# Kernel optimization log

Hardware: AMD Instinct MI355X
Metric: run time of the kernel (lower is better)

Reference implementation:

```python
import jax, jax.numpy as jnp
import numpy as np
import math

# model dims
B, S, T = 4, 256, 8
D_MODEL, D_STATE, N_HEAD, NUM_LAYERS = 256, 128, 4, 2
VOCAB = 32000
D_HEAD = D_STATE // N_HEAD
# AdaptiveLIFNeuron constants
TAU, BASE_THR, ADAPT, TARGET = 2.0, 1.0, 0.1, 0.02
DECAY = math.exp(-1.0 / TAU)


@jax.custom_vjp
def spike_fn(x):
    # spikingjelly surrogate.ATan forward = heaviside
    return (x >= 0).astype(x.dtype)

def _spike_fwd(x):
    return spike_fn(x), x

def _spike_bwd(x, g):
    # ATan surrogate gradient, alpha=2: 1 / (1 + (pi*x)^2)
    return (g / (1.0 + (math.pi * x) ** 2),)

spike_fn.defvjp(_spike_fwd, _spike_bwd)


def lif_step(x, v, thr):
    v_pot = v * DECAY + x
    spike = spike_fn(v_pot - jax.lax.stop_gradient(thr))
    v_new = v_pot * (1.0 - jax.lax.stop_gradient(spike))  # reset where spiked
    err = jax.lax.stop_gradient(spike.mean() - TARGET)    # torch.no_grad threshold update
    thr_new = jnp.maximum(thr + ADAPT * err, 0.5)
    return spike, v_new, thr_new


def ssm_layer(x_tbsd, A, C, Wq, bq, Wkv, bkv, Wo, bo):
    # x_tbsd: [T, B, S, d_model] spikes/embeddings, scanned over time
    scale = 1.0 / math.sqrt(D_HEAD)

    def step(carry, x_t):
        h, sv, ov, ts, to = carry
        st = h @ A.T                                      # [B,S,d_state]
        q = (h @ Wq.T + bq).reshape(B * S, N_HEAD, D_HEAD)
        kv = x_t @ Wkv.T + bkv                            # [B,S,2*d_state]
        k, v = jnp.split(kv, 2, axis=-1)
        k = k.reshape(B * S, N_HEAD, D_HEAD)
        v = v.reshape(B * S, N_HEAD, D_HEAD)
        # attention across all B*S positions (faithful to torch reshape)
        scores = jnp.einsum('ahd,bhd->hab', q, k) * scale  # [H, BS, BS]
        attn = jax.nn.softmax(scores, axis=-1)
        att = jnp.einsum('hab,bhd->ahd', attn, v).reshape(B, S, D_STATE)
        upd = st + att @ Wo.T + bo
        h2, sv2, ts2 = lif_step(upd, sv, ts)
        out_pot = h2 @ C.T                                 # [B,S,d_model]
        os_, ov2, to2 = lif_step(out_pot, ov, to)
        return (h2, sv2, ov2, ts2, to2), os_

    init = (jnp.zeros((B, S, D_STATE)), jnp.zeros((B, S, D_STATE)),
            jnp.zeros((B, S, D_MODEL)),
            jnp.full((D_STATE,), BASE_THR), jnp.full((D_MODEL,), BASE_THR))
    _, outs = jax.lax.scan(step, init, x_tbsd)
    return outs  # [T,B,S,d_model]


def setup_inputs() -> dict:
    key = jax.random.key(0)
    ks = jax.random.split(key, 8)
    nrm = lambda k, shape, s: jax.random.normal(k, shape, jnp.float32) * s
    L = NUM_LAYERS
    return {
        'input_ids': jax.random.randint(ks[0], (B, S), 0, VOCAB),
        'emb': nrm(ks[1], (VOCAB, D_MODEL), 0.02),
        'A': nrm(ks[2], (L, D_STATE, D_STATE), 1.0 / math.sqrt(D_STATE)),
        'C': nrm(ks[3], (L, D_MODEL, D_STATE), 1.0 / math.sqrt(D_STATE)),
        'Wq': nrm(ks[4], (L, D_STATE, D_STATE), 1.0 / math.sqrt(D_STATE)),
        'bq': jnp.zeros((L, D_STATE)),
        'Wkv': nrm(ks[5], (L, 2 * D_STATE, D_MODEL), 1.0 / math.sqrt(D_MODEL)),
        'bkv': jnp.zeros((L, 2 * D_STATE)),
        'Wo': nrm(ks[6], (L, D_STATE, D_STATE), 1.0 / math.sqrt(D_STATE)),
        'bo': jnp.zeros((L, D_STATE)),
        'Wout': nrm(ks[7], (VOCAB, D_MODEL), 1.0 / math.sqrt(D_MODEL)),
        'bout': jnp.zeros((VOCAB,)),
    }


def reference(input_ids, emb, A, C, Wq, bq, Wkv, bkv, Wo, bo, Wout, bout):
    tok = emb[input_ids]                                   # [B,S,d_model]
    # encoder_type='expand': replicate embedding over time steps
    hidden = jnp.broadcast_to(tok[None], (T, B, S, D_MODEL))
    for l in range(NUM_LAYERS):
        hidden = ssm_layer(hidden, A[l], C[l], Wq[l], bq[l],
                           Wkv[l], bkv[l], Wo[l], bo[l])
    time_integrated = hidden.mean(axis=0)                  # mean over time -> [B,S,d_model]
    logits = time_integrated @ Wout.T + bout               # output_projection -> [B,S,vocab]
    return logits
```

## Files before the change

### kernel.cpp

```cpp
#include <hip/hip_runtime.h>
#include <math.h>

#define BS_TOT   1024
#define DM       256
#define DST      128
#define TSTEPS   8
#define DECAYF   0.6065306597126334f
#define SCALEF   0.17677669529663689f
#define NE       (BS_TOT * DM)

__global__ void embed_k(const int* __restrict__ ids, const float* __restrict__ emb,
                        float* __restrict__ tok) {
    int r = blockIdx.x, c = threadIdx.x;
    tok[r * DM + c] = emb[(size_t)ids[r] * DM + c];
}

__global__ void prep_k(float* __restrict__ h, float* __restrict__ sv, float* __restrict__ ov,
                       float* __restrict__ W1T, float* __restrict__ WoT, float* __restrict__ CT,
                       const float* __restrict__ Al, const float* __restrict__ Wql,
                       const float* __restrict__ Wol, const float* __restrict__ Cl,
                       int* __restrict__ cnts) {
    int i = blockIdx.x * 256 + threadIdx.x;
    if (i < BS_TOT * DST) { h[i] = 0.f; sv[i] = 0.f; }
    ov[i] = 0.f;
    if (i < 32768) {
        int k = i >> 8, n = i & 255;
        W1T[i] = (n < 128) ? Al[n * 128 + k] : Wql[(n - 128) * 128 + k];
        CT[i]  = Cl[n * 128 + k];
    }
    if (i < 16384) {
        int k = i >> 7, n = i & 127;
        WoT[i] = Wol[n * 128 + k];
    }
    if (i < 16) cnts[i] = 0;
}

__global__ __launch_bounds__(256) void ktrans_k(const float* __restrict__ kv,
                                                float* __restrict__ kT) {
    __shared__ float tile[64][133];
    const float* src = kv + (size_t)blockIdx.y * NE;
    float* dst = kT + (size_t)blockIdx.y * (128 * 1024);
    const int kc = blockIdx.x, tid = threadIdx.x;
#pragma unroll
    for (int i = 0; i < 32; ++i) {
        int idx = i * 256 + tid;
        int key = idx >> 7, d = idx & 127;
        tile[key][d] = src[(size_t)(kc * 64 + key) * 256 + d];
    }
    __syncthreads();
#pragma unroll
    for (int i = 0; i < 32; ++i) {
        int idx = i * 256 + tid;
        int d = idx >> 6, key = idx & 63;
        dst[(size_t)d * 1024 + kc * 64 + key] = tile[key][d];
    }
}

__global__ void mean_k(const float* __restrict__ outs, float* __restrict__ ti) {
    int i = blockIdx.x * 256 + threadIdx.x;
    float s = 0.f;
#pragma unroll
    for (int t = 0; t < TSTEPS; ++t) s += outs[t * NE + i];
    ti[i] = s * 0.125f;
}

template <int BM, int BN, int BK, int TM, int TN>
__global__ __launch_bounds__((BM / TM) * (BN / TN))
void gemm_k(const float* __restrict__ Amat, const float* __restrict__ Wmat,
            const float* __restrict__ bias, float* __restrict__ outp,
            int M, int N, int K) {
    constexpr int NT  = (BM / TM) * (BN / TN);
    constexpr int NXT = BN / TN;
    __shared__ float As[BK][BM + 4];
    __shared__ float Bs[BK][BN + 4];
    const int tid = threadIdx.x;
    const int n0 = blockIdx.x * BN, m0 = blockIdx.y * BM;
    const int tx = tid % NXT, ty = tid / NXT;
    float acc[TM][TN] = {};

    for (int k0 = 0; k0 < K; k0 += BK) {
#pragma unroll
        for (int i = 0; i < (BM * BK) / NT; ++i) {
            int idx = i * NT + tid;
            int kk = idx % BK, mm = idx / BK;
            As[kk][mm] = Amat[(size_t)(m0 + mm) * K + k0 + kk];
        }
#pragma unroll
        for (int i = 0; i < (BN * BK) / NT; ++i) {
            int idx = i * NT + tid;
            int kk = idx % BK, nn = idx / BK;
            Bs[kk][nn] = Wmat[(size_t)(n0 + nn) * K + k0 + kk];
        }
        __syncthreads();
#pragma unroll
        for (int kk = 0; kk < BK; ++kk) {
            float a[TM], b[TN];
#pragma unroll
            for (int i = 0; i < TM; ++i) a[i] = As[kk][ty * TM + i];
#pragma unroll
            for (int j = 0; j < TN; ++j) b[j] = Bs[kk][tx * TN + j];
#pragma unroll
            for (int i = 0; i < TM; ++i)
#pragma unroll
                for (int j = 0; j < TN; ++j) acc[i][j] += a[i] * b[j];
        }
        __syncthreads();
    }
#pragma unroll
    for (int i = 0; i < TM; ++i) {
        int mr = m0 + ty * TM + i;
#pragma unroll
        for (int j = 0; j < TN; ++j) {
            int nc = n0 + tx * TN + j;
            float x = acc[i][j];
            if (bias) x += bias[nc];
            outp[(size_t)mr * N + nc] = x;
        }
    }
}

__global__ __launch_bounds__(256) void gemm_out_k(
    const float* __restrict__ Amat, const float* __restrict__ Wmat,
    const float* __restrict__ bias, float* __restrict__ outp)
{
    constexpr int BM = 128, BN = 128, BK = 16;
    constexpr int K = 256, N = 32000;
    __shared__ float As[BK][BM + 4];
    __shared__ float Bs[BK][BN + 4];
    const int tid = threadIdx.x;

    const int bid = blockIdx.x;
    const int g   = (bid & 7) * 250 + (bid >> 3);
    const int m0  = (g & 7) * BM;
    const int n0  = (g >> 3) * BN;

    const int tx = tid & 15, ty = tid >> 4;
    float acc[8][8] = {};

    for (int k0 = 0; k0 < K; k0 += BK) {
#pragma unroll
        for (int i = 0; i < 8; ++i) {
            int idx = i * 256 + tid;
            int kk = idx & 15, mm = idx >> 4;
            As[kk][mm] = Amat[(size_t)(m0 + mm) * K + k0 + kk];
        }
#pragma unroll
        for (int i = 0; i < 8; ++i) {
            int idx = i * 256 + tid;
            int kk = idx & 15, nn = idx >> 4;
            Bs[kk][nn] = Wmat[(size_t)(n0 + nn) * K + k0 + kk];
        }
        __syncthreads();
#pragma unroll
        for (int kk = 0; kk < BK; ++kk) {
            float a[8], b[8];
            *(float4*)&a[0] = *(const float4*)&As[kk][ty * 4];
            *(float4*)&a[4] = *(const float4*)&As[kk][64 + ty * 4];
            *(float4*)&b[0] = *(const float4*)&Bs[kk][tx * 4];
            *(float4*)&b[4] = *(const float4*)&Bs[kk][64 + tx * 4];
#pragma unroll
            for (int i = 0; i < 8; ++i)
#pragma unroll
                for (int j = 0; j < 8; ++j) acc[i][j] += a[i] * b[j];
        }
        __syncthreads();
    }

    float bv[8];
    *(float4*)&bv[0] = *(const float4*)&bias[n0 + tx * 4];
    *(float4*)&bv[4] = *(const float4*)&bias[n0 + 64 + tx * 4];
#pragma unroll
    for (int i = 0; i < 8; ++i) {
        const int mr = m0 + ((i < 4) ? (ty * 4 + i) : (64 + ty * 4 + i - 4));
        float4 o0, o1;
        o0.x = acc[i][0] + bv[0]; o0.y = acc[i][1] + bv[1];
        o0.z = acc[i][2] + bv[2]; o0.w = acc[i][3] + bv[3];
        o1.x = acc[i][4] + bv[4]; o1.y = acc[i][5] + bv[5];
        o1.z = acc[i][6] + bv[6]; o1.w = acc[i][7] + bv[7];
        float* dst = &outp[(size_t)mr * N + n0];
        *(float4*)(dst + tx * 4)      = o0;
        *(float4*)(dst + 64 + tx * 4) = o1;
    }
}

__global__ __launch_bounds__(256) void lif_k(
    const float* __restrict__ W1T,
    const float* __restrict__ WoT,
    const float* __restrict__ CT,
    const float* __restrict__ bq_w,
    const float* __restrict__ bo_w,
    float* __restrict__ h,
    float* __restrict__ sv,
    float* __restrict__ ov,
    const float* __restrict__ att_in,
    float* __restrict__ outs_prev,
    float* __restrict__ q_g,
    int* __restrict__ cnt1, int* __restrict__ cnt2, int t, int do_B)
{
    __shared__ float hA_s[4 * 128];
    __shared__ float h2_s[4 * 128];
    __shared__ float att_s[4 * 128];
    __shared__ unsigned long long umr_s[4][2];
    __shared__ unsigned long long um_s[2];
    __shared__ float thr_s[2];

    const int tid = threadIdx.x;
    const int r0 = blockIdx.x * 4;

    if (tid == 0) {
        float ts = 1.0f, to = 1.0f;
        for (int i = 0; i < t - 1; ++i) {
            float e1 = (float)cnt1[i] * (1.f / 131072.f) - 0.02f;
            ts = fmaxf(ts + 0.1f * e1, 0.5f);
            float e2 = (float)cnt2[i] * (1.f / 262144.f) - 0.02f;
            to = fmaxf(to + 0.1f * e2, 0.5f);
        }
        thr_s[0] = ts; thr_s[1] = to;
    }
    hA_s[tid]       = h[r0 * 128 + tid];
    hA_s[256 + tid] = h[r0 * 128 + 256 + tid];
    if (t > 0) {
        att_s[tid]       = att_in[r0 * 128 + tid];
        att_s[256 + tid] = att_in[r0 * 128 + 256 + tid];
    }
    __syncthreads();
    {
        int w = tid >> 6, l = tid & 63;
        unsigned long long b0 = __ballot(hA_s[w * 128 + l] != 0.f);
        unsigned long long b1 = __ballot(hA_s[w * 128 + 64 + l] != 0.f);
        if (l == 0) { umr_s[w][0] = b0; umr_s[w][1] = b1; }
    }
    __syncthreads();
    if (tid == 0) {
        um_s[0] = umr_s[0][0] | umr_s[1][0] | umr_s[2][0] | umr_s[3][0];
        um_s[1] = umr_s[0][1] | umr_s[1][1] | umr_s[2][1] | umr_s[3][1];
    }
    __syncthreads();

    const int n = tid & 127, half = tid >> 7;
    const int ra = half * 2, rb = half * 2 + 1;

    if (t > 0) {
        float sta = 0.f, stb = 0.f;
        unsigned long long u = um_s[0];
        while (u) {
            int k = __builtin_ctzll(u); u &= u - 1;
            float w = W1T[(k << 8) + n];
            sta += hA_s[ra * 128 + k] * w; stb += hA_s[rb * 128 + k] * w;
        }
        u = um_s[1];
        while (u) {
            int kk = __builtin_ctzll(u); u &= u - 1;
            int k = 64 + kk;
            float w = W1T[(k << 8) + n];
            sta += hA_s[ra * 128 + k] * w; stb += hA_s[rb * 128 + k] * w;
        }
        float ba = 0.f, bb = 0.f;
        for (int i4 = 0; i4 < 32; ++i4) {
            const int i = i4 * 4;
            float w0 = WoT[(i + 0) * 128 + n];
            float w1 = WoT[(i + 1) * 128 + n];
            float w2 = WoT[(i + 2) * 128 + n];
            float w3 = WoT[(i + 3) * 128 + n];
            float4 aa = *(const float4*)&att_s[ra * 128 + i];
            float4 ab = *(const float4*)&att_s[rb * 128 + i];
            ba += aa.x * w0; ba += aa.y * w1; ba += aa.z * w2; ba += aa.w * w3;
            bb += ab.x * w0; bb += ab.y * w1; bb += ab.z * w2; bb += ab.w * w3;
        }
        float ts = thr_s[0];
        float xa = ba + bo_w[n]; xa += sta;
        float va = sv[(r0 + ra) * 128 + n];
        float vpa = va * DECAYF + xa;
        float spa = (vpa - ts >= 0.f) ? 1.f : 0.f;
        h[(r0 + ra) * 128 + n]  = spa;
        sv[(r0 + ra) * 128 + n] = vpa * (1.f - spa);
        h2_s[ra * 128 + n] = spa;

        float xb = bb + bo_w[n]; xb += stb;
        float vb = sv[(r0 + rb) * 128 + n];
        float vpb = vb * DECAYF + xb;
        float spb = (vpb - ts >= 0.f) ? 1.f : 0.f;
        h[(r0 + rb) * 128 + n]  = spb;
        sv[(r0 + rb) * 128 + n] = vpb * (1.f - spb);
        h2_s[rb * 128 + n] = spb;

        unsigned long long bba = __ballot(spa != 0.f);
        unsigned long long bbb = __ballot(spb != 0.f);
        int w = tid >> 6, l = tid & 63;
        if (l == 0) {
            umr_s[ra][w & 1] = bba;
            umr_s[rb][w & 1] = bbb;
            atomicAdd(&cnt1[t - 1], __popcll(bba) + __popcll(bbb));
        }
    } else {
        h2_s[tid]       = hA_s[tid];
        h2_s[256 + tid] = hA_s[256 + tid];
    }
    __syncthreads();
    if (tid == 0) {
        um_s[0] = umr_s[0][0] | umr_s[1][0] | umr_s[2][0] | umr_s[3][0];
        um_s[1] = umr_s[0][1] | umr_s[1][1] | umr_s[2][1] | umr_s[3][1];
    }
    __syncthreads();

    if (t > 0) {
        const int n2 = tid;
        float a0 = 0.f, a1 = 0.f, a2 = 0.f, a3 = 0.f;
        unsigned long long u = um_s[0];
        while (u) {
            int k = __builtin_ctzll(u); u &= u - 1;
            float w = CT[(k << 8) + n2];
            a0 += h2_s[k] * w;       a1 += h2_s[128 + k] * w;
            a2 += h2_s[256 + k] * w; a3 += h2_s[384 + k] * w;
        }
        u = um_s[1];
        while (u) {
            int kk = __builtin_ctzll(u); u &= u - 1;
            int k = 64 + kk;
            float w = CT[(k << 8) + n2];
            a0 += h2_s[k] * w;       a1 += h2_s[128 + k] * w;
            a2 += h2_s[256 + k] * w; a3 += h2_s[384 + k] * w;
        }
        float to = thr_s[1];
        float accs[4] = {a0, a1, a2, a3};
        float sp[4];
#pragma unroll
        for (int r = 0; r < 4; ++r) {
            float vo = ov[(r0 + r) * 256 + n2];
            float vp = vo * DECAYF + accs[r];
            float s = (vp - to >= 0.f) ? 1.f : 0.f;
            sp[r] = s;
            outs_prev[(size_t)(r0 + r) * 256 + n2] = s;
            ov[(r0 + r) * 256 + n2] = vp * (1.f - s);
        }
        unsigned long long c0 = __ballot(sp[0] != 0.f);
        unsigned long long c1 = __ballot(sp[1] != 0.f);
        unsigned long long c2 = __ballot(sp[2] != 0.f);
        unsigned long long c3 = __ballot(sp[3] != 0.f);
        if ((tid & 63) == 0)
            atomicAdd(&cnt2[t - 1], __popcll(c0) + __popcll(c1) + __popcll(c2) + __popcll(c3));
    }

    if (do_B) {
        float qa = 0.f, qb = 0.f;
        unsigned long long u = um_s[0];
        while (u) {
            int k = __builtin_ctzll(u); u &= u - 1;
            float w = W1T[(k << 8) + 128 + n];
            qa += h2_s[ra * 128 + k] * w; qb += h2_s[rb * 128 + k] * w;
        }
        u = um_s[1];
        while (u) {
            int kk = __builtin_ctzll(u); u &= u - 1;
            int k = 64 + kk;
            float w = W1T[(k << 8) + 128 + n];
            qa += h2_s[ra * 128 + k] * w; qb += h2_s[rb * 128 + k] * w;
        }
        q_g[(r0 + ra) * 128 + n] = qa + bq_w[n];
        q_g[(r0 + rb) * 128 + n] = qb + bq_w[n];
    }
}

__global__ __launch_bounds__(256) void attn_k(
    const float* __restrict__ q_g,
    const float* __restrict__ kT,
    const float* __restrict__ kv,
    float* __restrict__ att_out)
{
    __shared__ float p_s[8][1032];
    __shared__ float v_s[2][64 * 32];
    __shared__ float q_s[8][32];
    __shared__ float red_s[8 * 33];
    __shared__ float mrow_s[8], linv_s[8];

    const int tid = threadIdx.x;
    const int hh = blockIdx.x >> 7;
    const int r0 = (blockIdx.x & 127) * 8;

    {
        int r = tid >> 5, d = tid & 31;
        q_s[r][d] = q_g[(size_t)(r0 + r) * 128 + hh * 32 + d];
    }
    __syncthreads();

    {
        const int w = tid >> 6, l = tid & 63;
        const int key4 = w * 64 + l;
        const float4* kT4 = (const float4*)(kT + (size_t)hh * 32 * 1024);
        float4 acc[8];
#pragma unroll
        for (int pass = 0; pass < 2; ++pass) {
            const int d0 = pass * 16;
            float4 kreg[16];
#pragma unroll
            for (int i = 0; i < 16; ++i) kreg[i] = kT4[(size_t)(d0 + i) * 256 + key4];
#pragma unroll
            for (int r = 0; r < 8; ++r)
                acc[r] = pass ? *(const float4*)&p_s[r][key4 * 4]
                              : make_float4(0.f, 0.f, 0.f, 0.f);
#pragma unroll
            for (int i4 = 0; i4 < 4; ++i4) {
#pragma unroll
                for (int r = 0; r < 8; ++r) {
                    float4 qv = *(const float4*)&q_s[r][d0 + i4 * 4];
                    float4 k0 = kreg[i4 * 4 + 0], k1 = kreg[i4 * 4 + 1];
                    float4 k2 = kreg[i4 * 4 + 2], k3 = kreg[i4 * 4 + 3];
                    acc[r].x += qv.x * k0.x; acc[r].x += qv.y * k1.x;
                    acc[r].x += qv.z * k2.x; acc[r].x += qv.w * k3.x;
                    acc[r].y += qv.x * k0.y; acc[r].y += qv.y * k1.y;
                    acc[r].y += qv.z * k2.y; acc[r].y += qv.w * k3.y;
                    acc[r].z += qv.x * k0.z; acc[r].z += qv.y * k1.z;
                    acc[r].z += qv.z * k2.z; acc[r].z += qv.w * k3.z;
                    acc[r].w += qv.x * k0.w; acc[r].w += qv.y * k1.w;
                    acc[r].w += qv.z * k2.w; acc[r].w += qv.w * k3.w;
                }
            }
            if (pass == 0) {
#pragma unroll
                for (int r = 0; r < 8; ++r)
                    *(float4*)&p_s[r][key4 * 4] = acc[r];
            } else {
#pragma unroll
                for (int r = 0; r < 8; ++r) {
                    acc[r].x *= SCALEF; acc[r].y *= SCALEF;
                    acc[r].z *= SCALEF; acc[r].w *= SCALEF;
                    *(float4*)&p_s[r][key4 * 4] = acc[r];
                }
            }
        }
    }
    __syncthreads();

    {
        const int rh = tid >> 5, lg = tid & 31;
        float mx = -1e30f;
        for (int jj = 0; jj < 32; ++jj) mx = fmaxf(mx, p_s[rh][lg + 32 * jj]);
        red_s[rh * 33 + lg] = mx;
        __syncthreads();
        if (tid < 8) {
            float m = red_s[tid * 33];
            for (int j = 1; j < 32; ++j) m = fmaxf(m, red_s[tid * 33 + j]);
            mrow_s[tid] = m;
        }
        __syncthreads();
        float m = mrow_s[rh];
        float ls = 0.f;
        for (int jj = 0; jj < 32; ++jj) {
            int a = lg + 32 * jj;
            float p = expf(p_s[rh][a] - m);
            p_s[rh][a] = p;
            ls += p;
        }
        red_s[rh * 33 + lg] = ls;
        __syncthreads();
        if (tid < 8) {
            float l = 0.f;
            for (int j = 0; j < 32; ++j) l += red_s[tid * 33 + j];
            linv_s[tid] = 1.0f / l;
        }
    }
    __syncthreads();

    {
        const int w = tid >> 6, l = tid & 63;
        const int r = l >> 3, dq = l & 7;
        const bool act = (w == 0);
        const float4* kv4 = (const float4*)kv;
        float4 stg0, stg1;
        {
            int i0 = tid, i1 = 256 + tid;
            stg0 = kv4[(size_t)(i0 >> 3) * 64 + 32 + hh * 8 + (i0 & 7)];
            stg1 = kv4[(size_t)(i1 >> 3) * 64 + 32 + hh * 8 + (i1 & 7)];
        }
        float4 a = make_float4(0.f, 0.f, 0.f, 0.f);
        for (int c = 0; c < 16; ++c) {
            float* vb = v_s[c & 1];
            *(float4*)&vb[tid * 4]        = stg0;
            *(float4*)&vb[1024 + tid * 4] = stg1;
            if (c < 15) {
                int i0 = tid, i1 = 256 + tid;
                stg0 = kv4[(size_t)((c + 1) * 64 + (i0 >> 3)) * 64 + 32 + hh * 8 + (i0 & 7)];
                stg1 = kv4[(size_t)((c + 1) * 64 + (i1 >> 3)) * 64 + 32 + hh * 8 + (i1 & 7)];
            }
            __syncthreads();
            if (act) {
#pragma unroll 4
                for (int k4 = 0; k4 < 16; ++k4) {
                    const int kb = k4 * 4;
                    float4 p4 = *(const float4*)&p_s[r][c * 64 + kb];
                    float4 v0 = *(const float4*)&vb[(kb + 0) * 32 + dq * 4];
                    float4 v1 = *(const float4*)&vb[(kb + 1) * 32 + dq * 4];
                    float4 v2 = *(const float4*)&vb[(kb + 2) * 32 + dq * 4];
                    float4 v3 = *(const float4*)&vb[(kb + 3) * 32 + dq * 4];
                    a.x += p4.x * v0.x; a.y += p4.x * v0.y; a.z += p4.x * v0.z; a.w += p4.x * v0.w;
                    a.x += p4.y * v1.x; a.y += p4.y * v1.y; a.z += p4.y * v1.z; a.w += p4.y * v1.w;
                    a.x += p4.z * v2.x; a.y += p4.z * v2.y; a.z += p4.z * v2.z; a.w += p4.z * v2.w;
                    a.x += p4.w * v3.x; a.y += p4.w * v3.y; a.z += p4.w * v3.z; a.w += p4.w * v3.w;
                }
            }
        }
        if (act) {
            float li = linv_s[r];
            a.x *= li; a.y *= li; a.z *= li; a.w *= li;
            *(float4*)&att_out[(size_t)(r0 + r) * 128 + hh * 32 + dq * 4] = a;
        }
    }
}

extern "C" void kernel_launch(void* const* d_in, const int* in_sizes, int n_in,
                              void* d_out, int out_size, void* d_ws, size_t ws_size,
                              hipStream_t stream) {
    (void)in_sizes; (void)n_in; (void)out_size; (void)ws_size;
    const int*   ids  = (const int*)d_in[0];
    const float* emb  = (const float*)d_in[1];
    const float* Aw   = (const float*)d_in[2];
    const float* Cw   = (const float*)d_in[3];
    const float* Wq   = (const float*)d_in[4];
    const float* bq   = (const float*)d_in[5];
    const float* Wkv  = (const float*)d_in[6];
    const float* bkv  = (const float*)d_in[7];
    const float* Wo   = (const float*)d_in[8];
    const float* bo   = (const float*)d_in[9];
    const float* Wout = (const float*)d_in[10];
    const float* bout = (const float*)d_in[11];
    float* out = (float*)d_out;
    float* ws  = (float*)d_ws;

    float* tok  = ws;
    float* bufA = tok  + NE;
    float* bufB = bufA + 8 * NE;
    float* kvb  = bufB + 8 * NE;
    float* kTb  = kvb  + 8 * NE;
    float* attb = kTb  + 8 * 131072;
    float* hbuf = attb + 131072;
    float* svb  = hbuf + 131072;
    float* ovb  = svb  + 131072;
    float* qg   = ovb  + 262144;
    float* ti   = qg   + 131072;
    float* W1T  = ti   + NE;
    float* WoT  = W1T  + 32768;
    float* CT   = WoT  + 16384;
    int*   cnts = (int*)(CT + 32768);

    embed_k<<<dim3(1024), dim3(256), 0, stream>>>(ids, emb, tok);

    for (int l = 0; l < 2; ++l) {
        const float* Al   = Aw  + l * 16384;
        const float* Cl   = Cw  + l * 32768;
        const float* Wql  = Wq  + l * 16384;
        const float* bql  = bq  + l * 128;
        const float* Wkvl = Wkv + l * 65536;
        const float* bkvl = bkv + l * 256;
        const float* Wol  = Wo  + l * 16384;
        const float* bol  = bo  + l * 128;
        const float* xin  = (l == 0) ? tok : bufA;
        float* outs       = (l == 0) ? bufA : bufB;
        const int Mkv     = (l == 0) ? BS_TOT : 8 * BS_TOT;
        const int nt      = (l == 0) ? 1 : 8;

        prep_k<<<dim3(1024), dim3(256), 0, stream>>>(hbuf, svb, ovb, W1T, WoT, CT,
                                                     Al, Wql, Wol, Cl, cnts);

        gemm_k<64, 64, 16, 4, 4><<<dim3(256 / 64, Mkv / 64), dim3(256), 0, stream>>>(
            xin, Wkvl, bkvl, kvb, Mkv, 256, 256);

        ktrans_k<<<dim3(16, nt), dim3(256), 0, stream>>>(kvb, kTb);

        for (int t = 0; t <= TSTEPS; ++t) {
            const int do_B = (t < TSTEPS) ? 1 : 0;
            float* outs_prev = outs + (size_t)((t > 0) ? (t - 1) : 0) * NE;
            lif_k<<<dim3(256), dim3(256), 0, stream>>>(
                W1T, WoT, CT, bql, bol,
                hbuf, svb, ovb, attb, outs_prev, qg,
                cnts, cnts + 8, t, do_B);
            if (do_B) {
                const float* kT_t = (l == 0) ? kTb : kTb + (size_t)t * 131072;
                const float* kv_t = (l == 0) ? kvb : kvb + (size_t)t * NE;
                attn_k<<<dim3(512), dim3(256), 0, stream>>>(qg, kT_t, kv_t, attb);
            }
        }
    }

    mean_k<<<dim3(1024), dim3(256), 0, stream>>>(bufB, ti);

    gemm_out_k<<<dim3(2000), dim3(256), 0, stream>>>(ti, Wout, bout, out);
}
```

Before: 1.271 ms.

## Double-buffer output GEMM and software-pipeline sparse spike-driven matvec loops

The vocab output GEMM now uses two shared-memory buffers and register prefetch, so global loads for the next K tile overlap the FMA work on the current tile, and one barrier per iteration is removed. The sparse bitmask-driven loops in the recurrent kernel load the next weight one iteration ahead to hide memory latency. The C and Wq sparse products are merged into a single loop over the active mask so it is walked once. The cost is more registers and shared memory, which may lower occupancy, and the merged loop now runs even when t==0 or do_B is false.

```diff
diff --git a/kernel.cpp b/kernel.cpp
--- a/kernel.cpp
+++ b/kernel.cpp
@@ -125,8 +125,8 @@
 {
     constexpr int BM = 128, BN = 128, BK = 16;
     constexpr int K = 256, N = 32000;
-    __shared__ float As[BK][BM + 4];
-    __shared__ float Bs[BK][BN + 4];
+    __shared__ float As[2][BK][BM + 4];
+    __shared__ float Bs[2][BK][BN + 4];
     const int tid = threadIdx.x;
 
     const int bid = blockIdx.x;
@@ -136,34 +136,59 @@
 
     const int tx = tid & 15, ty = tid >> 4;
     float acc[8][8] = {};
-
-    for (int k0 = 0; k0 < K; k0 += BK) {
-#pragma unroll
-        for (int i = 0; i < 8; ++i) {
-            int idx = i * 256 + tid;
-            int kk = idx & 15, mm = idx >> 4;
-            As[kk][mm] = Amat[(size_t)(m0 + mm) * K + k0 + kk];
-        }
-#pragma unroll
-        for (int i = 0; i < 8; ++i) {
-            int idx = i * 256 + tid;
-            int kk = idx & 15, nn = idx >> 4;
-            Bs[kk][nn] = Wmat[(size_t)(n0 + nn) * K + k0 + kk];
-        }
-        __syncthreads();
+    float ra_[8], rb_[8];
+
+#pragma unroll
+    for (int i = 0; i < 8; ++i) {
+        int idx = i * 256 + tid;
+        int kk = idx & 15, mm = idx >> 4;
+        ra_[i] = Amat[(size_t)(m0 + mm) * K + kk];
+        rb_[i] = Wmat[(size_t)(n0 + mm) * K + kk];
+    }
+#pragma unroll
+    for (int i = 0; i < 8; ++i) {
+        int idx = i * 256 + tid;
+        int kk = idx & 15, mm = idx >> 4;
+        As[0][kk][mm] = ra_[i];
+        Bs[0][kk][mm] = rb_[i];
+    }
+    __syncthreads();
+
+    int p = 0;
+    for (int k0 = BK; k0 <= K; k0 += BK) {
+        const bool pf = (k0 < K);
+        if (pf) {
+#pragma unroll
+            for (int i = 0; i < 8; ++i) {
+                int idx = i * 256 + tid;
+                int kk = idx & 15, mm = idx >> 4;
+                ra_[i] = Amat[(size_t)(m0 + mm) * K + k0 + kk];
+                rb_[i] = Wmat[(size_t)(n0 + mm) * K + k0 + kk];
+            }
+        }
 #pragma unroll
         for (int kk = 0; kk < BK; ++kk) {
             float a[8], b[8];
-            *(float4*)&a[0] = *(const float4*)&As[kk][ty * 4];
-            *(float4*)&a[4] = *(const float4*)&As[kk][64 + ty * 4];
-            *(float4*)&b[0] = *(const float4*)&Bs[kk][tx * 4];
-            *(float4*)&b[4] = *(const float4*)&Bs[kk][64 + tx * 4];
+            *(float4*)&a[0] = *(const float4*)&As[p][kk][ty * 4];
+            *(float4*)&a[4] = *(const float4*)&As[p][kk][64 + ty * 4];
+            *(float4*)&b[0] = *(const float4*)&Bs[p][kk][tx * 4];
+            *(float4*)&b[4] = *(const float4*)&Bs[p][kk][64 + tx * 4];
 #pragma unroll
             for (int i = 0; i < 8; ++i)
 #pragma unroll
                 for (int j = 0; j < 8; ++j) acc[i][j] += a[i] * b[j];
         }
-        __syncthreads();
+        if (pf) {
+#pragma unroll
+            for (int i = 0; i < 8; ++i) {
+                int idx = i * 256 + tid;
+                int kk = idx & 15, mm = idx >> 4;
+                As[p ^ 1][kk][mm] = ra_[i];
+                Bs[p ^ 1][kk][mm] = rb_[i];
+            }
+            __syncthreads();
+            p ^= 1;
+        }
     }
 
     float bv[8];
@@ -242,18 +267,27 @@
 
     if (t > 0) {
         float sta = 0.f, stb = 0.f;
-        unsigned long long u = um_s[0];
-        while (u) {
-            int k = __builtin_ctzll(u); u &= u - 1;
-            float w = W1T[(k << 8) + n];
-            sta += hA_s[ra * 128 + k] * w; stb += hA_s[rb * 128 + k] * w;
-        }
-        u = um_s[1];
-        while (u) {
-            int kk = __builtin_ctzll(u); u &= u - 1;
-            int k = 64 + kk;
-            float w = W1T[(k << 8) + n];
-            sta += hA_s[ra * 128 + k] * w; stb += hA_s[rb * 128 + k] * w;
+        {
+            unsigned long long u = um_s[0];
+            int kp = 0; float wp = 0.f; bool have = (u != 0ull);
+            if (have) { kp = __builtin_ctzll(u); u &= u - 1; wp = W1T[(kp << 8) + n]; }
+            while (u) {
+                int kn = __builtin_ctzll(u); u &= u - 1;
+                float wn = W1T[(kn << 8) + n];
+                sta += hA_s[ra * 128 + kp] * wp; stb += hA_s[rb * 128 + kp] * wp;
+                kp = kn; wp = wn;
+            }
+            if (have) { sta += hA_s[ra * 128 + kp] * wp; stb += hA_s[rb * 128 + kp] * wp; }
+            u = um_s[1];
+            have = (u != 0ull);
+            if (have) { kp = 64 + __builtin_ctzll(u); u &= u - 1; wp = W1T[(kp << 8) + n]; }
+            while (u) {
+                int kn = 64 + __builtin_ctzll(u); u &= u - 1;
+                float wn = W1T[(kn << 8) + n];
+                sta += hA_s[ra * 128 + kp] * wp; stb += hA_s[rb * 128 + kp] * wp;
+                kp = kn; wp = wn;
+            }
+            if (have) { sta += hA_s[ra * 128 + kp] * wp; stb += hA_s[rb * 128 + kp] * wp; }
         }
         float ba = 0.f, bb = 0.f;
         for (int i4 = 0; i4 < 32; ++i4) {
@@ -303,61 +337,75 @@
     }
     __syncthreads();
 
-    if (t > 0) {
+    {
         const int n2 = tid;
-        float a0 = 0.f, a1 = 0.f, a2 = 0.f, a3 = 0.f;
+        float a0 = 0.f, a1 = 0.f, a2 = 0.f, a3 = 0.f, qa = 0.f, qb = 0.f;
         unsigned long long u = um_s[0];
+        int kp = 0; float wc = 0.f, wq = 0.f; bool have = (u != 0ull);
+        if (have) {
+            kp = __builtin_ctzll(u); u &= u - 1;
+            wc = CT[(kp << 8) + n2]; wq = W1T[(kp << 8) + 128 + n];
+        }
         while (u) {
-            int k = __builtin_ctzll(u); u &= u - 1;
-            float w = CT[(k << 8) + n2];
-            a0 += h2_s[k] * w;       a1 += h2_s[128 + k] * w;
-            a2 += h2_s[256 + k] * w; a3 += h2_s[384 + k] * w;
+            int kn = __builtin_ctzll(u); u &= u - 1;
+            float wcn = CT[(kn << 8) + n2];
+            float wqn = W1T[(kn << 8) + 128 + n];
+            a0 += h2_s[kp] * wc;       a1 += h2_s[128 + kp] * wc;
+            a2 += h2_s[256 + kp] * wc; a3 += h2_s[384 + kp] * wc;
+            qa += h2_s[ra * 128 + kp] * wq; qb += h2_s[rb * 128 + kp] * wq;
+            kp = kn; wc = wcn; wq = wqn;
+        }
+        if (have) {
+            a0 += h2_s[kp] * wc;       a1 += h2_s[128 + kp] * wc;
+            a2 += h2_s[256 + kp] * wc; a3 += h2_s[384 + kp] * wc;
+            qa += h2_s[ra * 128 + kp] * wq; qb += h2_s[rb * 128 + kp] * wq;
         }
         u = um_s[1];
+        have = (u != 0ull);
+        if (have) {
+            kp = 64 + __builtin_ctzll(u); u &= u - 1;
+            wc = CT[(kp << 8) + n2]; wq = W1T[(kp << 8) + 128 + n];
+        }
         while (u) {
-            int kk = __builtin_ctzll(u); u &= u - 1;
-            int k = 64 + kk;
-            float w = CT[(k << 8) + n2];
-            a0 += h2_s[k] * w;       a1 += h2_s[128 + k] * w;
-            a2 += h2_s[256 + k] * w; a3 += h2_s[384 + k] * w;
-        }
-        float to = thr_s[1];
-        float accs[4] = {a0, a1, a2, a3};
-        float sp[4];
-#pragma unroll
-        for (int r = 0; r < 4; ++r) {
-            float vo = ov[(r0 + r) * 256 + n2];
-            float vp = vo * DECAYF + accs[r];
-            float s = (vp - to >= 0.f) ? 1.f : 0.f;
-            sp[r] = s;
-            outs_prev[(size_t)(r0 + r) * 256 + n2] = s;
-            ov[(r0 + r) * 256 + n2] = vp * (1.f - s);
-        }
-        unsigned long long c0 = __ballot(sp[0] != 0.f);
-        unsigned long long c1 = __ballot(sp[1] != 0.f);
-        unsigned long long c2 = __ballot(sp[2] != 0.f);
-        unsigned long long c3 = __ballot(sp[3] != 0.f);
-        if ((tid & 63) == 0)
-            atomicAdd(&cnt2[t - 1], __popcll(c0) + __popcll(c1) + __popcll(c2) + __popcll(c3));
-    }
-
-    if (do_B) {
-        float qa = 0.f, qb = 0.f;
-        unsigned long long u = um_s[0];
-        while (u) {
-            int k = __builtin_ctzll(u); u &= u - 1;
-            float w = W1T[(k << 8) + 128 + n];
-            qa += h2_s[ra * 128 + k] * w; qb += h2_s[rb * 128 + k] * w;
-        }
-        u = um_s[1];
-        while (u) {
-            int kk = __builtin_ctzll(u); u &= u - 1;
-            int k = 64 + kk;
-            float w = W1T[(k << 8) + 128 + n];
-            qa += h2_s[ra * 128 + k] * w; qb += h2_s[rb * 128 + k] * w;
-        }
-        q_g[(r0 + ra) * 128 + n] = qa + bq_w[n];
-        q_g[(r0 + rb) * 128 + n] = qb + bq_w[n];
+            int kn = 64 + __builtin_ctzll(u); u &= u - 1;
+            float wcn = CT[(kn << 8) + n2];
+            float wqn = W1T[(kn << 8) + 128 + n];
+            a0 += h2_s[kp] * wc;       a1 += h2_s[128 + kp] * wc;
+            a2 += h2_s[256 + kp] * wc; a3 += h2_s[384 + kp] * wc;
+            qa += h2_s[ra * 128 + kp] * wq; qb += h2_s[rb * 128 + kp] * wq;
+            kp = kn; wc = wcn; wq = wqn;
+        }
+        if (have) {
+            a0 += h2_s[kp] * wc;       a1 += h2_s[128 + kp] * wc;
+            a2 += h2_s[256 + kp] * wc; a3 += h2_s[384 + kp] * wc;
+            qa += h2_s[ra * 128 + kp] * wq; qb += h2_s[rb * 128 + kp] * wq;
+        }
+
+        if (t > 0) {
+            float to = thr_s[1];
+            float accs[4] = {a0, a1, a2, a3};
+            float sp[4];
+#pragma unroll
+            for (int r = 0; r < 4; ++r) {
+                float vo = ov[(r0 + r) * 256 + n2];
+                float vp = vo * DECAYF + accs[r];
+                float s = (vp - to >= 0.f) ? 1.f : 0.f;
+                sp[r] = s;
+                outs_prev[(size_t)(r0 + r) * 256 + n2] = s;
+                ov[(r0 + r) * 256 + n2] = vp * (1.f - s);
+            }
+            unsigned long long c0 = __ballot(sp[0] != 0.f);
+            unsigned long long c1 = __ballot(sp[1] != 0.f);
+            unsigned long long c2 = __ballot(sp[2] != 0.f);
+            unsigned long long c3 = __ballot(sp[3] != 0.f);
+            if ((tid & 63) == 0)
+                atomicAdd(&cnt2[t - 1], __popcll(c0) + __popcll(c1) + __popcll(c2) + __popcll(c3));
+        }
+
+        if (do_B) {
+            q_g[(r0 + ra) * 128 + n] = qa + bq_w[n];
+            q_g[(r0 + rb) * 128 + n] = qb + bq_w[n];
+        }
     }
 }
 
```

Result: slower. 1.395 ms (+9.8%).

## Use direct global-to-LDS loads with swizzle in vocab GEMM; spread P·V over two waves

Applied to the files above, without the earlier changes.

The output-projection GEMM now stages A and W tiles with global_load_lds 16-byte direct-to-LDS transfers into a K-contiguous, XOR-swizzled layout with BK=32, replacing the register-staged transposed stores. The inner loop reads float4 along K and unpacks four k-steps at a time. Separately, the attention P·V accumulation now uses two waves with two outputs per thread instead of one wave with four, to raise parallelism in that phase. The swizzle is meant to avoid LDS bank conflicts, but the loads are still not double-buffered.

```diff
diff --git a/kernel.cpp b/kernel.cpp
--- a/kernel.cpp
+++ b/kernel.cpp
@@ -8,6 +8,11 @@
 #define DECAYF   0.6065306597126334f
 #define SCALEF   0.17677669529663689f
 #define NE       (BS_TOT * DM)
+
+#define GLOAD_LDS16(g, l) \
+    __builtin_amdgcn_global_load_lds( \
+        (const __attribute__((address_space(1))) void*)(g), \
+        (__attribute__((address_space(3))) void*)(l), 16, 0, 0)
 
 __global__ void embed_k(const int* __restrict__ ids, const float* __restrict__ emb,
                         float* __restrict__ tok) {
@@ -123,45 +128,60 @@
     const float* __restrict__ Amat, const float* __restrict__ Wmat,
     const float* __restrict__ bias, float* __restrict__ outp)
 {
-    constexpr int BM = 128, BN = 128, BK = 16;
     constexpr int K = 256, N = 32000;
-    __shared__ float As[BK][BM + 4];
-    __shared__ float Bs[BK][BN + 4];
+    __shared__ float As2[128 * 32];
+    __shared__ float Bs2[128 * 32];
     const int tid = threadIdx.x;
 
     const int bid = blockIdx.x;
     const int g   = (bid & 7) * 250 + (bid >> 3);
-    const int m0  = (g & 7) * BM;
-    const int n0  = (g >> 3) * BN;
+    const int m0  = (g & 7) * 128;
+    const int n0  = (g >> 3) * 128;
 
     const int tx = tid & 15, ty = tid >> 4;
     float acc[8][8] = {};
 
-    for (int k0 = 0; k0 < K; k0 += BK) {
-#pragma unroll
-        for (int i = 0; i < 8; ++i) {
+    const int swa = ty & 7;
+    const int swb = tx & 7;
+
+    for (int k0 = 0; k0 < K; k0 += 32) {
+#pragma unroll
+        for (int i = 0; i < 4; ++i) {
             int idx = i * 256 + tid;
-            int kk = idx & 15, mm = idx >> 4;
-            As[kk][mm] = Amat[(size_t)(m0 + mm) * K + k0 + kk];
-        }
-#pragma unroll
-        for (int i = 0; i < 8; ++i) {
-            int idx = i * 256 + tid;
-            int kk = idx & 15, nn = idx >> 4;
-            Bs[kk][nn] = Wmat[(size_t)(n0 + nn) * K + k0 + kk];
+            int row = idx >> 3, k4 = idx & 7;
+            int k4s = k4 ^ ((row >> 2) & 7);
+            GLOAD_LDS16(&Amat[(size_t)(m0 + row) * K + k0 + k4s * 4], &As2[idx * 4]);
+            GLOAD_LDS16(&Wmat[(size_t)(n0 + row) * K + k0 + k4s * 4], &Bs2[idx * 4]);
         }
         __syncthreads();
-#pragma unroll
-        for (int kk = 0; kk < BK; ++kk) {
-            float a[8], b[8];
-            *(float4*)&a[0] = *(const float4*)&As[kk][ty * 4];
-            *(float4*)&a[4] = *(const float4*)&As[kk][64 + ty * 4];
-            *(float4*)&b[0] = *(const float4*)&Bs[kk][tx * 4];
-            *(float4*)&b[4] = *(const float4*)&Bs[kk][64 + tx * 4];
-#pragma unroll
-            for (int i = 0; i < 8; ++i)
-#pragma unroll
-                for (int j = 0; j < 8; ++j) acc[i][j] += a[i] * b[j];
+
+#pragma unroll
+        for (int kg = 0; kg < 8; ++kg) {
+            const int pa = (kg ^ swa) * 4;
+            const int pb = (kg ^ swb) * 4;
+            float4 a0[4], a1[4], b0[4], b1[4];
+#pragma unroll
+            for (int i = 0; i < 4; ++i) {
+                a0[i] = *(const float4*)&As2[(ty * 4 + i) * 32 + pa];
+                a1[i] = *(const float4*)&As2[(64 + ty * 4 + i) * 32 + pa];
+                b0[i] = *(const float4*)&Bs2[(tx * 4 + i) * 32 + pb];
+                b1[i] = *(const float4*)&Bs2[(64 + tx * 4 + i) * 32 + pb];
+            }
+#pragma unroll
+            for (int kk2 = 0; kk2 < 4; ++kk2) {
+                float a[8], b[8];
+#pragma unroll
+                for (int i = 0; i < 4; ++i) {
+                    a[i]     = ((const float*)&a0[i])[kk2];
+                    a[4 + i] = ((const float*)&a1[i])[kk2];
+                    b[i]     = ((const float*)&b0[i])[kk2];
+                    b[4 + i] = ((const float*)&b1[i])[kk2];
+                }
+#pragma unroll
+                for (int i = 0; i < 8; ++i)
+#pragma unroll
+                    for (int j = 0; j < 8; ++j) acc[i][j] += a[i] * b[j];
+            }
         }
         __syncthreads();
     }
@@ -463,8 +483,9 @@
 
     {
         const int w = tid >> 6, l = tid & 63;
-        const int r = l >> 3, dq = l & 7;
-        const bool act = (w == 0);
+        const int r = (w & 1) * 4 + (l >> 4);
+        const int dp = l & 15;
+        const bool act = (w < 2);
         const float4* kv4 = (const float4*)kv;
         float4 stg0, stg1;
         {
@@ -472,7 +493,7 @@
             stg0 = kv4[(size_t)(i0 >> 3) * 64 + 32 + hh * 8 + (i0 & 7)];
             stg1 = kv4[(size_t)(i1 >> 3) * 64 + 32 + hh * 8 + (i1 & 7)];
         }
-        float4 a = make_float4(0.f, 0.f, 0.f, 0.f);
+        float a0 = 0.f, a1 = 0.f;
         for (int c = 0; c < 16; ++c) {
             float* vb = v_s[c & 1];
             *(float4*)&vb[tid * 4]        = stg0;
@@ -488,21 +509,21 @@
                 for (int k4 = 0; k4 < 16; ++k4) {
                     const int kb = k4 * 4;
                     float4 p4 = *(const float4*)&p_s[r][c * 64 + kb];
-                    float4 v0 = *(const float4*)&vb[(kb + 0) * 32 + dq * 4];
-                    float4 v1 = *(const float4*)&vb[(kb + 1) * 32 + dq * 4];
-                    float4 v2 = *(const float4*)&vb[(kb + 2) * 32 + dq * 4];
-                    float4 v3 = *(const float4*)&vb[(kb + 3) * 32 + dq * 4];
-                    a.x += p4.x * v0.x; a.y += p4.x * v0.y; a.z += p4.x * v0.z; a.w += p4.x * v0.w;
-                    a.x += p4.y * v1.x; a.y += p4.y * v1.y; a.z += p4.y * v1.z; a.w += p4.y * v1.w;
-                    a.x += p4.z * v2.x; a.y += p4.z * v2.y; a.z += p4.z * v2.z; a.w += p4.z * v2.w;
-                    a.x += p4.w * v3.x; a.y += p4.w * v3.y; a.z += p4.w * v3.z; a.w += p4.w * v3.w;
+                    float2 v0 = *(const float2*)&vb[(kb + 0) * 32 + 2 * dp];
+                    float2 v1 = *(const float2*)&vb[(kb + 1) * 32 + 2 * dp];
+                    float2 v2 = *(const float2*)&vb[(kb + 2) * 32 + 2 * dp];
+                    float2 v3 = *(const float2*)&vb[(kb + 3) * 32 + 2 * dp];
+                    a0 += p4.x * v0.x; a1 += p4.x * v0.y;
+                    a0 += p4.y * v1.x; a1 += p4.y * v1.y;
+                    a0 += p4.z * v2.x; a1 += p4.z * v2.y;
+                    a0 += p4.w * v3.x; a1 += p4.w * v3.y;
                 }
             }
         }
         if (act) {
             float li = linv_s[r];
-            a.x *= li; a.y *= li; a.z *= li; a.w *= li;
-            *(float4*)&att_out[(size_t)(r0 + r) * 128 + hh * 32 + dq * 4] = a;
+            *(float2*)&att_out[(size_t)(r0 + r) * 128 + hh * 32 + 2 * dp] =
+                make_float2(a0 * li, a1 * li);
         }
     }
 }
```

Result: no change. 1.295 ms (+1.9%).

## Widen output GEMM K-tile with float4 loads and spread attention PV across two waves

Applied to the files above, without the earlier changes.

The vocab projection GEMM now uses a K tile of 32 and loads A and W tiles with float4 global reads, halving the number of K iterations and barriers. In the attention kernel, QK accumulators stay in registers across both passes instead of round-tripping through shared memory. The PV stage now runs on two waves, each thread producing two outputs, using a single padded V buffer with an extra barrier per chunk in place of double buffering. Shared memory per GEMM block roughly doubles, and the added barrier may expose the global load latency for V.

```diff
diff --git a/kernel.cpp b/kernel.cpp
--- a/kernel.cpp
+++ b/kernel.cpp
@@ -123,7 +123,7 @@
     const float* __restrict__ Amat, const float* __restrict__ Wmat,
     const float* __restrict__ bias, float* __restrict__ outp)
 {
-    constexpr int BM = 128, BN = 128, BK = 16;
+    constexpr int BM = 128, BN = 128, BK = 32;
     constexpr int K = 256, N = 32000;
     __shared__ float As[BK][BM + 4];
     __shared__ float Bs[BK][BN + 4];
@@ -139,16 +139,15 @@
 
     for (int k0 = 0; k0 < K; k0 += BK) {
 #pragma unroll
-        for (int i = 0; i < 8; ++i) {
+        for (int i = 0; i < 4; ++i) {
             int idx = i * 256 + tid;
-            int kk = idx & 15, mm = idx >> 4;
-            As[kk][mm] = Amat[(size_t)(m0 + mm) * K + k0 + kk];
-        }
-#pragma unroll
-        for (int i = 0; i < 8; ++i) {
-            int idx = i * 256 + tid;
-            int kk = idx & 15, nn = idx >> 4;
-            Bs[kk][nn] = Wmat[(size_t)(n0 + nn) * K + k0 + kk];
+            int mm = idx >> 3, k4 = idx & 7;
+            float4 va = *(const float4*)&Amat[(size_t)(m0 + mm) * K + k0 + k4 * 4];
+            As[k4 * 4 + 0][mm] = va.x; As[k4 * 4 + 1][mm] = va.y;
+            As[k4 * 4 + 2][mm] = va.z; As[k4 * 4 + 3][mm] = va.w;
+            float4 vb = *(const float4*)&Wmat[(size_t)(n0 + mm) * K + k0 + k4 * 4];
+            Bs[k4 * 4 + 0][mm] = vb.x; Bs[k4 * 4 + 1][mm] = vb.y;
+            Bs[k4 * 4 + 2][mm] = vb.z; Bs[k4 * 4 + 3][mm] = vb.w;
         }
         __syncthreads();
 #pragma unroll
@@ -368,7 +367,7 @@
     float* __restrict__ att_out)
 {
     __shared__ float p_s[8][1032];
-    __shared__ float v_s[2][64 * 32];
+    __shared__ float v_s[64 * 36];
     __shared__ float q_s[8][32];
     __shared__ float red_s[8 * 33];
     __shared__ float mrow_s[8], linv_s[8];
@@ -389,15 +388,13 @@
         const float4* kT4 = (const float4*)(kT + (size_t)hh * 32 * 1024);
         float4 acc[8];
 #pragma unroll
+        for (int r = 0; r < 8; ++r) acc[r] = make_float4(0.f, 0.f, 0.f, 0.f);
+#pragma unroll
         for (int pass = 0; pass < 2; ++pass) {
             const int d0 = pass * 16;
             float4 kreg[16];
 #pragma unroll
             for (int i = 0; i < 16; ++i) kreg[i] = kT4[(size_t)(d0 + i) * 256 + key4];
-#pragma unroll
-            for (int r = 0; r < 8; ++r)
-                acc[r] = pass ? *(const float4*)&p_s[r][key4 * 4]
-                              : make_float4(0.f, 0.f, 0.f, 0.f);
 #pragma unroll
             for (int i4 = 0; i4 < 4; ++i4) {
 #pragma unroll
@@ -415,18 +412,12 @@
                     acc[r].w += qv.z * k2.w; acc[r].w += qv.w * k3.w;
                 }
             }
-            if (pass == 0) {
-#pragma unroll
-                for (int r = 0; r < 8; ++r)
-                    *(float4*)&p_s[r][key4 * 4] = acc[r];
-            } else {
-#pragma unroll
-                for (int r = 0; r < 8; ++r) {
-                    acc[r].x *= SCALEF; acc[r].y *= SCALEF;
-                    acc[r].z *= SCALEF; acc[r].w *= SCALEF;
-                    *(float4*)&p_s[r][key4 * 4] = acc[r];
-                }
-            }
+        }
+#pragma unroll
+        for (int r = 0; r < 8; ++r) {
+            acc[r].x *= SCALEF; acc[r].y *= SCALEF;
+            acc[r].z *= SCALEF; acc[r].w *= SCALEF;
+            *(float4*)&p_s[r][key4 * 4] = acc[r];
         }
     }
     __syncthreads();
@@ -463,8 +454,9 @@
 
     {
         const int w = tid >> 6, l = tid & 63;
-        const int r = l >> 3, dq = l & 7;
-        const bool act = (w == 0);
+        const int r = (w & 1) * 4 + (l >> 4);
+        const int dp = l & 15;
+        const bool act = (w < 2);
         const float4* kv4 = (const float4*)kv;
         float4 stg0, stg1;
         {
@@ -472,11 +464,13 @@
             stg0 = kv4[(size_t)(i0 >> 3) * 64 + 32 + hh * 8 + (i0 & 7)];
             stg1 = kv4[(size_t)(i1 >> 3) * 64 + 32 + hh * 8 + (i1 & 7)];
         }
-        float4 a = make_float4(0.f, 0.f, 0.f, 0.f);
+        float a0 = 0.f, a1 = 0.f;
         for (int c = 0; c < 16; ++c) {
-            float* vb = v_s[c & 1];
-            *(float4*)&vb[tid * 4]        = stg0;
-            *(float4*)&vb[1024 + tid * 4] = stg1;
+            {
+                int i0 = tid, i1 = 256 + tid;
+                *(float4*)&v_s[(i0 >> 3) * 36 + (i0 & 7) * 4] = stg0;
+                *(float4*)&v_s[(i1 >> 3) * 36 + (i1 & 7) * 4] = stg1;
+            }
             if (c < 15) {
                 int i0 = tid, i1 = 256 + tid;
                 stg0 = kv4[(size_t)((c + 1) * 64 + (i0 >> 3)) * 64 + 32 + hh * 8 + (i0 & 7)];
@@ -488,21 +482,22 @@
                 for (int k4 = 0; k4 < 16; ++k4) {
                     const int kb = k4 * 4;
                     float4 p4 = *(const float4*)&p_s[r][c * 64 + kb];
-                    float4 v0 = *(const float4*)&vb[(kb + 0) * 32 + dq * 4];
-                    float4 v1 = *(const float4*)&vb[(kb + 1) * 32 + dq * 4];
-                    float4 v2 = *(const float4*)&vb[(kb + 2) * 32 + dq * 4];
-                    float4 v3 = *(const float4*)&vb[(kb + 3) * 32 + dq * 4];
-                    a.x += p4.x * v0.x; a.y += p4.x * v0.y; a.z += p4.x * v0.z; a.w += p4.x * v0.w;
-                    a.x += p4.y * v1.x; a.y += p4.y * v1.y; a.z += p4.y * v1.z; a.w += p4.y * v1.w;
-                    a.x += p4.z * v2.x; a.y += p4.z * v2.y; a.z += p4.z * v2.z; a.w += p4.z * v2.w;
-                    a.x += p4.w * v3.x; a.y += p4.w * v3.y; a.z += p4.w * v3.z; a.w += p4.w * v3.w;
+                    float2 v0 = *(const float2*)&v_s[(kb + 0) * 36 + 2 * dp];
+                    float2 v1 = *(const float2*)&v_s[(kb + 1) * 36 + 2 * dp];
+                    float2 v2 = *(const float2*)&v_s[(kb + 2) * 36 + 2 * dp];
+                    float2 v3 = *(const float2*)&v_s[(kb + 3) * 36 + 2 * dp];
+                    a0 += p4.x * v0.x; a1 += p4.x * v0.y;
+                    a0 += p4.y * v1.x; a1 += p4.y * v1.y;
+                    a0 += p4.z * v2.x; a1 += p4.z * v2.y;
+                    a0 += p4.w * v3.x; a1 += p4.w * v3.y;
                 }
             }
+            __syncthreads();
         }
         if (act) {
             float li = linv_s[r];
-            a.x *= li; a.y *= li; a.z *= li; a.w *= li;
-            *(float4*)&att_out[(size_t)(r0 + r) * 128 + hh * 32 + dq * 4] = a;
+            *(float2*)&att_out[(size_t)(r0 + r) * 128 + hh * 32 + 2 * dp] =
+                make_float2(a0 * li, a1 * li);
         }
     }
 }
```

New measurement: 1.241 ms, median of 2. 2.3% less time.
